# Performance work log

Hardware: AMD Instinct MI355X
Metric: run time of the kernel (lower is better)

## Reference

```python
import jax, jax.numpy as jnp
import numpy as np

SEQ, H, NC = 20, 128, 100000

def _lstm_cell(x, h, c, Wih, Whh, bih, bhh):
    # gates: [B, 4H] in PyTorch order i, f, g, o
    g = x @ Wih.T + bih + h @ Whh.T + bhh
    i, f, gg, o = jnp.split(g, 4, axis=-1)
    c2 = jax.nn.sigmoid(f) * c + jax.nn.sigmoid(i) * jnp.tanh(gg)
    h2 = jax.nn.sigmoid(o) * jnp.tanh(c2)
    return h2, c2

def setup_inputs() -> dict:
    key = jax.random.key(0)
    ks = jax.random.split(key, 24)
    u = lambda k, shp, bound: jax.random.uniform(k, shp, jnp.float32, -bound, bound)
    s1 = 1.0 / np.sqrt(H)       # PyTorch LSTMCell init bound, hidden_size=H
    s2 = 1.0 / np.sqrt(2 * H)   # combined cell, hidden_size=2H
    kn = lambda k, shp: jax.random.normal(k, shp, jnp.float32) * np.sqrt(2.0 / shp[1])  # kaiming_normal_
    return {
        'x': jax.random.normal(ks[0], (SEQ, 1, H), jnp.float32),
        'h0f': kn(ks[1], (1, H)), 'c0f': kn(ks[2], (1, H)),
        'h0b': kn(ks[3], (1, H)), 'c0b': kn(ks[4], (1, H)),
        'h0l': kn(ks[5], (1, 2 * H)), 'c0l': kn(ks[6], (1, 2 * H)),
        'Wih_f': u(ks[7], (4 * H, H), s1), 'Whh_f': u(ks[8], (4 * H, H), s1),
        'bih_f': u(ks[9], (4 * H,), s1), 'bhh_f': u(ks[10], (4 * H,), s1),
        'Wih_b': u(ks[11], (4 * H, H), s1), 'Whh_b': u(ks[12], (4 * H, H), s1),
        'bih_b': u(ks[13], (4 * H,), s1), 'bhh_b': u(ks[14], (4 * H,), s1),
        'Wih_l': u(ks[15], (8 * H, 2 * H), s2), 'Whh_l': u(ks[16], (8 * H, 2 * H), s2),
        'bih_l': u(ks[17], (8 * H,), s2), 'bhh_l': u(ks[18], (8 * H,), s2),
        'Wlin': u(ks[19], (NC, 2 * H), 1.0 / np.sqrt(2 * H)),
        'blin': u(ks[20], (NC,), 1.0 / np.sqrt(2 * H)),
    }

def reference(x, h0f, c0f, h0b, c0b, h0l, c0l,
              Wih_f, Whh_f, bih_f, bhh_f,
              Wih_b, Whh_b, bih_b, bhh_b,
              Wih_l, Whh_l, bih_l, bhh_l,
              Wlin, blin):
    xs = x.reshape(SEQ, 1, H)

    def step_f(carry, xt):
        h, c = _lstm_cell(xt, carry[0], carry[1], Wih_f, Whh_f, bih_f, bhh_f)
        return (h, c), h
    _, fwd = jax.lax.scan(step_f, (h0f, c0f), xs)          # [SEQ, 1, H]

    def step_b(carry, xt):
        h, c = _lstm_cell(xt, carry[0], carry[1], Wih_b, Whh_b, bih_b, bhh_b)
        return (h, c), h
    # backward list is kept in reversed-scan order (NOT flipped back), per source zip
    _, bwd = jax.lax.scan(step_b, (h0b, c0b), xs[::-1])    # [SEQ, 1, H]

    comb = jnp.concatenate([fwd, bwd], axis=-1)            # [SEQ, 1, 2H]

    def step_l(carry, xt):
        h, c = _lstm_cell(xt, carry[0], carry[1], Wih_l, Whh_l, bih_l, bhh_l)
        return (h, c), h
    _, hl = jax.lax.scan(step_l, (h0l, c0l), comb)         # [SEQ, 1, 2H]

    fb = hl.reshape(SEQ, 2 * H)
    return fb @ Wlin.T + blin                              # [SEQ, NC]
```

## Files before the change

### kernel.cpp

```cpp
#include <hip/hip_runtime.h>
#include <stdint.h>

#define SEQ  20
#define H1   128
#define H2   256
#define NCLS 100000

__device__ __forceinline__ float sigm(float x) { return 1.0f / (1.0f + __expf(-x)); }
__device__ __forceinline__ float tanhfast(float x) {
    float e = __expf(-2.0f * fabsf(x));
    float t = (1.0f - e) / (1.0f + e);
    return copysignf(t, x);
}

__device__ __forceinline__ void gbar(int* cnt, int target) {
    __syncthreads();
    if (threadIdx.x == 0) {
        __hip_atomic_fetch_add(cnt, 1, __ATOMIC_ACQ_REL, __HIP_MEMORY_SCOPE_AGENT);
        while (__hip_atomic_load(cnt, __ATOMIC_ACQUIRE, __HIP_MEMORY_SCOPE_AGENT) < target)
            __builtin_amdgcn_s_sleep(2);
    }
    __syncthreads();
}

__global__ __launch_bounds__(256, 1) void k_l1g(
    const float* __restrict__ x,
    const float* __restrict__ h0f, const float* __restrict__ c0f,
    const float* __restrict__ h0b, const float* __restrict__ c0b,
    const float* __restrict__ WihF, const float* __restrict__ WhhF,
    const float* __restrict__ bihF, const float* __restrict__ bhhF,
    const float* __restrict__ WihB, const float* __restrict__ WhhB,
    const float* __restrict__ bihB, const float* __restrict__ bhhB,
    float* __restrict__ comb,
    float* __restrict__ hg,
    int* __restrict__ sync)
{
    const int b   = blockIdx.x;
    const int dir = b >> 3, sub = b & 7;
    const float* Wih = dir ? WihB : WihF;
    const float* Whh = dir ? WhhB : WhhF;
    const float* bih = dir ? bihB : bihF;
    const float* bhh = dir ? bhhB : bhhF;
    const float* h0  = dir ? h0b  : h0f;
    const float* c0  = dir ? c0b  : c0f;

    __shared__ float whhS[64 * 129];
    __shared__ float gxs[64][SEQ];
    __shared__ float xs[H1];
    __shared__ float partial[4 * 64];
    __shared__ float hcur[H1];
    __shared__ float gv[64];

    const int tid = threadIdx.x;
    const int lr  = tid & 63;
    const int q   = tid >> 6;

    float biasv = 0.0f;
    if (tid < 64) {
        int R = (tid >> 4) * H1 + sub * 16 + (tid & 15);
        biasv = bih[R] + bhh[R];
    }
    {
        int r2 = tid >> 2, sg = tid & 3;
        int R = (r2 >> 4) * H1 + sub * 16 + (r2 & 15);
        const float* src = Whh + R * H1 + sg * 32;
        float* dst = whhS + r2 * 129 + sg * 32;
        for (int i = 0; i < 32; ++i) dst[i] = src[i];
    }
    if (tid < H1) hcur[tid] = h0[tid];
    float cst = 0.0f;
    if (tid < 16) cst = c0[sub * 16 + tid];
    __syncthreads();

    for (int t = 0; t < SEQ; ++t) {
        int tx = dir ? (SEQ - 1 - t) : t;
        if (tid < H1) xs[tid] = x[tx * H1 + tid];
        __syncthreads();
        {
            int R = (lr >> 4) * H1 + sub * 16 + (lr & 15);
            const float* wp = Wih + R * H1 + q * 32;
            const float* xp = xs + q * 32;
            float a = 0.0f;
#pragma unroll
            for (int k = 0; k < 32; k += 4) {
                float4 wv = *(const float4*)(wp + k);
                a += wv.x * xp[k] + wv.y * xp[k + 1] + wv.z * xp[k + 2] + wv.w * xp[k + 3];
            }
            partial[q * 64 + lr] = a;
        }
        __syncthreads();
        if (tid < 64)
            gxs[tid][t] = biasv + partial[tid] + partial[64 + tid]
                        + partial[128 + tid] + partial[192 + tid];
        __syncthreads();
    }

    for (int t = 0; t < SEQ; ++t) {
        {
            const float* wp = whhS + lr * 129 + q * 32;
            const float* hp = hcur + q * 32;
            float a = 0.0f;
#pragma unroll
            for (int k = 0; k < 32; ++k) a += wp[k] * hp[k];
            partial[q * 64 + lr] = a;
        }
        __syncthreads();
        if (tid < 64)
            gv[tid] = gxs[tid][t] + partial[tid] + partial[64 + tid]
                    + partial[128 + tid] + partial[192 + tid];
        __syncthreads();
        if (tid < 16) {
            float gi = gv[tid], gf = gv[16 + tid], gg = gv[32 + tid], go = gv[48 + tid];
            float cn = sigm(gf) * cst + sigm(gi) * tanhfast(gg);
            cst = cn;
            float hn = sigm(go) * tanhfast(cn);
            comb[t * H2 + dir * H1 + sub * 16 + tid] = hn;
            __hip_atomic_store(&hg[dir * H1 + sub * 16 + tid], hn,
                               __ATOMIC_RELEASE, __HIP_MEMORY_SCOPE_AGENT);
        }
        gbar(&sync[dir], 8 * (t + 1));
        if (tid < H1)
            hcur[tid] = __hip_atomic_load(&hg[dir * H1 + tid],
                                          __ATOMIC_RELAXED, __HIP_MEMORY_SCOPE_AGENT);
        __syncthreads();
    }
}

__global__ __launch_bounds__(256, 1) void k_l2g(
    const float* __restrict__ Whhl,
    const float* __restrict__ h0l, const float* __restrict__ c0l,
    const float* __restrict__ Wihl,
    const float* __restrict__ bihl, const float* __restrict__ bhhl,
    const float* __restrict__ comb,
    float* __restrict__ fb,
    float* __restrict__ hg2,
    int* __restrict__ sync)
{
    const int b = blockIdx.x;
    __shared__ float whhS[32 * 257];
    __shared__ float gxs[32][SEQ];
    __shared__ float combt[H2];
    __shared__ float partial[8 * 32];
    __shared__ float hcur[H2];
    __shared__ float gv[32];

    const int tid = threadIdx.x;
    const int lr  = tid & 31;
    const int q   = tid >> 5;
    const int c0  = b * 8;

    float biasv = 0.0f;
    if (tid < 32) {
        int R = (tid >> 3) * H2 + c0 + (tid & 7);
        biasv = bihl[R] + bhhl[R];
    }
    {
        int r2 = tid >> 3, sg = tid & 7;
        int R = (r2 >> 3) * H2 + c0 + (r2 & 7);
        const float* src = Whhl + R * H2 + sg * 32;
        float* dst = whhS + r2 * 257 + sg * 32;
        for (int i = 0; i < 32; ++i) dst[i] = src[i];
    }
    if (tid < H2) hcur[tid] = h0l[tid];
    float cst = 0.0f;
    if (tid < 8) cst = c0l[c0 + tid];
    __syncthreads();

    for (int t = 0; t < SEQ; ++t) {
        combt[tid] = comb[t * H2 + tid];
        __syncthreads();
        {
            int R = (lr >> 3) * H2 + c0 + (lr & 7);
            const float* wp = Wihl + R * H2 + q * 32;
            const float* cp = combt + q * 32;
            float a = 0.0f;
#pragma unroll
            for (int k = 0; k < 32; k += 4) {
                float4 wv = *(const float4*)(wp + k);
                a += wv.x * cp[k] + wv.y * cp[k + 1] + wv.z * cp[k + 2] + wv.w * cp[k + 3];
            }
            partial[q * 32 + lr] = a;
        }
        __syncthreads();
        if (tid < 32) {
            float s = biasv;
#pragma unroll
            for (int qq = 0; qq < 8; ++qq) s += partial[qq * 32 + tid];
            gxs[tid][t] = s;
        }
        __syncthreads();
    }

    for (int t = 0; t < SEQ; ++t) {
        {
            const float* wp = whhS + lr * 257 + q * 32;
            const float* hp = hcur + q * 32;
            float a = 0.0f;
#pragma unroll
            for (int k = 0; k < 32; ++k) a += wp[k] * hp[k];
            partial[q * 32 + lr] = a;
        }
        __syncthreads();
        if (tid < 32) {
            float s = gxs[tid][t];
#pragma unroll
            for (int qq = 0; qq < 8; ++qq) s += partial[qq * 32 + tid];
            gv[tid] = s;
        }
        __syncthreads();
        if (tid < 8) {
            float gi = gv[tid], gf = gv[8 + tid], gg = gv[16 + tid], go = gv[24 + tid];
            float cn = sigm(gf) * cst + sigm(gi) * tanhfast(gg);
            cst = cn;
            float hn = sigm(go) * tanhfast(cn);
            fb[t * H2 + c0 + tid] = hn;
            __hip_atomic_store(&hg2[c0 + tid], hn,
                               __ATOMIC_RELEASE, __HIP_MEMORY_SCOPE_AGENT);
        }
        gbar(&sync[2], 32 * (t + 1));
        hcur[tid] = __hip_atomic_load(&hg2[tid],
                                      __ATOMIC_RELAXED, __HIP_MEMORY_SCOPE_AGENT);
        __syncthreads();
    }
}

__global__ __launch_bounds__(256, 4) void k_out_v(
    const float* __restrict__ Wlin, const float* __restrict__ blin,
    const float* __restrict__ fb, float* __restrict__ out)
{
    __shared__ float fbs[H2][SEQ];
    const int tid = threadIdx.x;
    for (int t = 0; t < SEQ; ++t) fbs[tid][t] = fb[t * H2 + tid];
    __syncthreads();

    int n = blockIdx.x * 256 + tid;
    if (n >= NCLS) return;
    float acc[SEQ];
    float bv = blin[n];
#pragma unroll
    for (int t = 0; t < SEQ; ++t) acc[t] = bv;

    const float* wp = Wlin + (size_t)n * H2;
    for (int k = 0; k < H2; k += 4) {
        float4 wv = *(const float4*)(wp + k);
#pragma unroll
        for (int t = 0; t < SEQ; t += 4) {
            float4 f0 = *(const float4*)(&fbs[k][t]);
            float4 f1 = *(const float4*)(&fbs[k + 1][t]);
            float4 f2 = *(const float4*)(&fbs[k + 2][t]);
            float4 f3 = *(const float4*)(&fbs[k + 3][t]);
            acc[t]     += wv.x * f0.x + wv.y * f1.x + wv.z * f2.x + wv.w * f3.x;
            acc[t + 1] += wv.x * f0.y + wv.y * f1.y + wv.z * f2.y + wv.w * f3.y;
            acc[t + 2] += wv.x * f0.z + wv.y * f1.z + wv.z * f2.z + wv.w * f3.z;
            acc[t + 3] += wv.x * f0.w + wv.y * f1.w + wv.z * f2.w + wv.w * f3.w;
        }
    }
#pragma unroll
    for (int t = 0; t < SEQ; ++t)
        out[(size_t)t * NCLS + n] = acc[t];
}

extern "C" void kernel_launch(void* const* d_in, const int* in_sizes, int n_in,
                              void* d_out, int out_size, void* d_ws, size_t ws_size,
                              hipStream_t stream)
{
    const float* x    = (const float*)d_in[0];
    const float* h0f_ = (const float*)d_in[1];
    const float* c0f_ = (const float*)d_in[2];
    const float* h0b_ = (const float*)d_in[3];
    const float* c0b_ = (const float*)d_in[4];
    const float* h0l_ = (const float*)d_in[5];
    const float* c0l_ = (const float*)d_in[6];
    const float* WihF = (const float*)d_in[7];
    const float* WhhF = (const float*)d_in[8];
    const float* bihF = (const float*)d_in[9];
    const float* bhhF = (const float*)d_in[10];
    const float* WihB = (const float*)d_in[11];
    const float* WhhB = (const float*)d_in[12];
    const float* bihB = (const float*)d_in[13];
    const float* bhhB = (const float*)d_in[14];
    const float* Wihl = (const float*)d_in[15];
    const float* Whhl = (const float*)d_in[16];
    const float* bihl = (const float*)d_in[17];
    const float* bhhl = (const float*)d_in[18];
    const float* Wlin = (const float*)d_in[19];
    const float* blin = (const float*)d_in[20];

    char* ws = (char*)d_ws;
    int*   sync = (int*)ws;
    float* hg   = (float*)(ws + 256);
    float* hg2  = (float*)(ws + 1536);
    float* comb = (float*)(ws + 4096);
    float* fb   = (float*)(ws + 24576);

    hipMemsetAsync(sync, 0, 256, stream);

    k_l1g<<<16, 256, 0, stream>>>(x, h0f_, c0f_, h0b_, c0b_,
                                  WihF, WhhF, bihF, bhhF,
                                  WihB, WhhB, bihB, bhhB,
                                  comb, hg, sync);
    k_l2g<<<32, 256, 0, stream>>>(Whhl, h0l_, c0l_,
                                  Wihl, bihl, bhhl,
                                  comb, fb, hg2, sync);
    k_out_v<<<391, 256, 0, stream>>>(Wlin, blin, fb, (float*)d_out);
}
```

Measured before the change: 358.0 us.

## Collapse LSTM layers to fewer blocks with register-resident weights

```diff
diff --git a/kernel.cpp b/kernel.cpp
--- a/kernel.cpp
+++ b/kernel.cpp
@@ -18,12 +18,12 @@
     if (threadIdx.x == 0) {
         __hip_atomic_fetch_add(cnt, 1, __ATOMIC_ACQ_REL, __HIP_MEMORY_SCOPE_AGENT);
         while (__hip_atomic_load(cnt, __ATOMIC_ACQUIRE, __HIP_MEMORY_SCOPE_AGENT) < target)
-            __builtin_amdgcn_s_sleep(2);
-    }
-    __syncthreads();
-}
-
-__global__ __launch_bounds__(256, 1) void k_l1g(
+            __builtin_amdgcn_s_sleep(1);
+    }
+    __syncthreads();
+}
+
+__global__ __launch_bounds__(512, 2) void k_l1r(
     const float* __restrict__ x,
     const float* __restrict__ h0f, const float* __restrict__ c0f,
     const float* __restrict__ h0b, const float* __restrict__ c0b,
@@ -31,12 +31,9 @@
     const float* __restrict__ bihF, const float* __restrict__ bhhF,
     const float* __restrict__ WihB, const float* __restrict__ WhhB,
     const float* __restrict__ bihB, const float* __restrict__ bhhB,
-    float* __restrict__ comb,
-    float* __restrict__ hg,
-    int* __restrict__ sync)
-{
-    const int b   = blockIdx.x;
-    const int dir = b >> 3, sub = b & 7;
+    float* __restrict__ comb)
+{
+    const int dir = blockIdx.x;
     const float* Wih = dir ? WihB : WihF;
     const float* Whh = dir ? WhhB : WhhF;
     const float* bih = dir ? bihB : bihF;
@@ -44,89 +41,73 @@
     const float* h0  = dir ? h0b  : h0f;
     const float* c0  = dir ? c0b  : c0f;
 
-    __shared__ float whhS[64 * 129];
-    __shared__ float gxs[64][SEQ];
-    __shared__ float xs[H1];
-    __shared__ float partial[4 * 64];
+    __shared__ float xs[SEQ * H1];
     __shared__ float hcur[H1];
-    __shared__ float gv[64];
+    __shared__ float gv[4 * H1];
+    __shared__ float gxs[4 * H1][SEQ + 1];
 
     const int tid = threadIdx.x;
-    const int lr  = tid & 63;
-    const int q   = tid >> 6;
-
-    float biasv = 0.0f;
-    if (tid < 64) {
-        int R = (tid >> 4) * H1 + sub * 16 + (tid & 15);
-        biasv = bih[R] + bhh[R];
-    }
-    {
-        int r2 = tid >> 2, sg = tid & 3;
-        int R = (r2 >> 4) * H1 + sub * 16 + (r2 & 15);
-        const float* src = Whh + R * H1 + sg * 32;
-        float* dst = whhS + r2 * 129 + sg * 32;
-        for (int i = 0; i < 32; ++i) dst[i] = src[i];
-    }
+
+    for (int i = tid; i < SEQ * H1; i += 512) xs[i] = x[i];
     if (tid < H1) hcur[tid] = h0[tid];
-    float cst = 0.0f;
-    if (tid < 16) cst = c0[sub * 16 + tid];
-    __syncthreads();
-
-    for (int t = 0; t < SEQ; ++t) {
-        int tx = dir ? (SEQ - 1 - t) : t;
-        if (tid < H1) xs[tid] = x[tx * H1 + tid];
-        __syncthreads();
-        {
-            int R = (lr >> 4) * H1 + sub * 16 + (lr & 15);
-            const float* wp = Wih + R * H1 + q * 32;
-            const float* xp = xs + q * 32;
-            float a = 0.0f;
-#pragma unroll
-            for (int k = 0; k < 32; k += 4) {
-                float4 wv = *(const float4*)(wp + k);
-                a += wv.x * xp[k] + wv.y * xp[k + 1] + wv.z * xp[k + 2] + wv.w * xp[k + 3];
-            }
-            partial[q * 64 + lr] = a;
-        }
-        __syncthreads();
-        if (tid < 64)
-            gxs[tid][t] = biasv + partial[tid] + partial[64 + tid]
-                        + partial[128 + tid] + partial[192 + tid];
-        __syncthreads();
-    }
-
-    for (int t = 0; t < SEQ; ++t) {
-        {
-            const float* wp = whhS + lr * 129 + q * 32;
-            const float* hp = hcur + q * 32;
-            float a = 0.0f;
-#pragma unroll
-            for (int k = 0; k < 32; ++k) a += wp[k] * hp[k];
-            partial[q * 64 + lr] = a;
-        }
-        __syncthreads();
-        if (tid < 64)
-            gv[tid] = gxs[tid][t] + partial[tid] + partial[64 + tid]
-                    + partial[128 + tid] + partial[192 + tid];
-        __syncthreads();
-        if (tid < 16) {
-            float gi = gv[tid], gf = gv[16 + tid], gg = gv[32 + tid], go = gv[48 + tid];
-            float cn = sigm(gf) * cst + sigm(gi) * tanhfast(gg);
-            cst = cn;
+    float creg = (tid < H1) ? c0[tid] : 0.0f;
+    const float bias = bih[tid] + bhh[tid];
+
+    float w[H1];
+    {
+        const float* wr = Wih + tid * H1;
+#pragma unroll
+        for (int k = 0; k < H1; k += 4) {
+            float4 v = *(const float4*)(wr + k);
+            w[k] = v.x; w[k + 1] = v.y; w[k + 2] = v.z; w[k + 3] = v.w;
+        }
+    }
+    __syncthreads();
+
+    for (int t = 0; t < SEQ; ++t) {
+        const float* xp = xs + (dir ? (SEQ - 1 - t) : t) * H1;
+        float a0 = 0.f, a1 = 0.f, a2 = 0.f, a3 = 0.f;
+#pragma unroll
+        for (int k = 0; k < H1; k += 4) {
+            float4 hv = *(const float4*)(xp + k);
+            a0 += w[k] * hv.x; a1 += w[k + 1] * hv.y;
+            a2 += w[k + 2] * hv.z; a3 += w[k + 3] * hv.w;
+        }
+        gxs[tid][t] = bias + ((a0 + a1) + (a2 + a3));
+    }
+
+    {
+        const float* wr = Whh + tid * H1;
+#pragma unroll
+        for (int k = 0; k < H1; k += 4) {
+            float4 v = *(const float4*)(wr + k);
+            w[k] = v.x; w[k + 1] = v.y; w[k + 2] = v.z; w[k + 3] = v.w;
+        }
+    }
+
+    for (int t = 0; t < SEQ; ++t) {
+        float a0 = 0.f, a1 = 0.f, a2 = 0.f, a3 = 0.f;
+#pragma unroll
+        for (int k = 0; k < H1; k += 4) {
+            float4 hv = *(const float4*)(hcur + k);
+            a0 += w[k] * hv.x; a1 += w[k + 1] * hv.y;
+            a2 += w[k + 2] * hv.z; a3 += w[k + 3] * hv.w;
+        }
+        gv[tid] = gxs[tid][t] + ((a0 + a1) + (a2 + a3));
+        __syncthreads();
+        if (tid < H1) {
+            float gi = gv[tid], gf = gv[H1 + tid], gg = gv[2 * H1 + tid], go = gv[3 * H1 + tid];
+            float cn = sigm(gf) * creg + sigm(gi) * tanhfast(gg);
+            creg = cn;
             float hn = sigm(go) * tanhfast(cn);
-            comb[t * H2 + dir * H1 + sub * 16 + tid] = hn;
-            __hip_atomic_store(&hg[dir * H1 + sub * 16 + tid], hn,
-                               __ATOMIC_RELEASE, __HIP_MEMORY_SCOPE_AGENT);
-        }
-        gbar(&sync[dir], 8 * (t + 1));
-        if (tid < H1)
-            hcur[tid] = __hip_atomic_load(&hg[dir * H1 + tid],
-                                          __ATOMIC_RELAXED, __HIP_MEMORY_SCOPE_AGENT);
-        __syncthreads();
-    }
-}
-
-__global__ __launch_bounds__(256, 1) void k_l2g(
+            comb[t * H2 + dir * H1 + tid] = hn;
+            hcur[tid] = hn;
+        }
+        __syncthreads();
+    }
+}
+
+__global__ __launch_bounds__(512, 2) void k_l2r(
     const float* __restrict__ Whhl,
     const float* __restrict__ h0l, const float* __restrict__ c0l,
     const float* __restrict__ Wihl,
@@ -137,89 +118,81 @@
     int* __restrict__ sync)
 {
     const int b = blockIdx.x;
-    __shared__ float whhS[32 * 257];
-    __shared__ float gxs[32][SEQ];
-    __shared__ float combt[H2];
-    __shared__ float partial[8 * 32];
+    __shared__ float cs[SEQ * H2];
     __shared__ float hcur[H2];
-    __shared__ float gv[32];
-
-    const int tid = threadIdx.x;
-    const int lr  = tid & 31;
-    const int q   = tid >> 5;
-    const int c0  = b * 8;
-
-    float biasv = 0.0f;
-    if (tid < 32) {
-        int R = (tid >> 3) * H2 + c0 + (tid & 7);
-        biasv = bihl[R] + bhhl[R];
-    }
-    {
-        int r2 = tid >> 3, sg = tid & 7;
-        int R = (r2 >> 3) * H2 + c0 + (r2 & 7);
-        const float* src = Whhl + R * H2 + sg * 32;
-        float* dst = whhS + r2 * 257 + sg * 32;
-        for (int i = 0; i < 32; ++i) dst[i] = src[i];
-    }
+    __shared__ float gv[4 * 64];
+    __shared__ float gxs[H2][SEQ + 1];
+
+    const int tid  = threadIdx.x;
+    const int L    = tid >> 1;
+    const int half = tid & 1;
+    const int R    = (L >> 6) * H2 + b * 64 + (L & 63);
+    const float bias = bihl[R] + bhhl[R];
+
+    for (int i = tid; i < SEQ * H2; i += 512) cs[i] = comb[i];
     if (tid < H2) hcur[tid] = h0l[tid];
-    float cst = 0.0f;
-    if (tid < 8) cst = c0l[c0 + tid];
-    __syncthreads();
-
-    for (int t = 0; t < SEQ; ++t) {
-        combt[tid] = comb[t * H2 + tid];
-        __syncthreads();
-        {
-            int R = (lr >> 3) * H2 + c0 + (lr & 7);
-            const float* wp = Wihl + R * H2 + q * 32;
-            const float* cp = combt + q * 32;
-            float a = 0.0f;
-#pragma unroll
-            for (int k = 0; k < 32; k += 4) {
-                float4 wv = *(const float4*)(wp + k);
-                a += wv.x * cp[k] + wv.y * cp[k + 1] + wv.z * cp[k + 2] + wv.w * cp[k + 3];
-            }
-            partial[q * 32 + lr] = a;
-        }
-        __syncthreads();
-        if (tid < 32) {
-            float s = biasv;
-#pragma unroll
-            for (int qq = 0; qq < 8; ++qq) s += partial[qq * 32 + tid];
-            gxs[tid][t] = s;
-        }
-        __syncthreads();
-    }
-
-    for (int t = 0; t < SEQ; ++t) {
-        {
-            const float* wp = whhS + lr * 257 + q * 32;
-            const float* hp = hcur + q * 32;
-            float a = 0.0f;
-#pragma unroll
-            for (int k = 0; k < 32; ++k) a += wp[k] * hp[k];
-            partial[q * 32 + lr] = a;
-        }
-        __syncthreads();
-        if (tid < 32) {
-            float s = gxs[tid][t];
-#pragma unroll
-            for (int qq = 0; qq < 8; ++qq) s += partial[qq * 32 + tid];
-            gv[tid] = s;
-        }
-        __syncthreads();
-        if (tid < 8) {
-            float gi = gv[tid], gf = gv[8 + tid], gg = gv[16 + tid], go = gv[24 + tid];
-            float cn = sigm(gf) * cst + sigm(gi) * tanhfast(gg);
-            cst = cn;
+    float creg = (tid < 64) ? c0l[b * 64 + tid] : 0.0f;
+
+    float w[H1];
+    {
+        const float* wr = Wihl + R * H2 + half * H1;
+#pragma unroll
+        for (int k = 0; k < H1; k += 4) {
+            float4 v = *(const float4*)(wr + k);
+            w[k] = v.x; w[k + 1] = v.y; w[k + 2] = v.z; w[k + 3] = v.w;
+        }
+    }
+    __syncthreads();
+
+    for (int t = 0; t < SEQ; ++t) {
+        const float* cp = cs + t * H2 + half * H1;
+        float a0 = 0.f, a1 = 0.f, a2 = 0.f, a3 = 0.f;
+#pragma unroll
+        for (int k = 0; k < H1; k += 4) {
+            float4 hv = *(const float4*)(cp + k);
+            a0 += w[k] * hv.x; a1 += w[k + 1] * hv.y;
+            a2 += w[k + 2] * hv.z; a3 += w[k + 3] * hv.w;
+        }
+        float a = (a0 + a1) + (a2 + a3);
+        a += __shfl_xor(a, 1);
+        if (half == 0) gxs[L][t] = bias + a;
+    }
+
+    {
+        const float* wr = Whhl + R * H2 + half * H1;
+#pragma unroll
+        for (int k = 0; k < H1; k += 4) {
+            float4 v = *(const float4*)(wr + k);
+            w[k] = v.x; w[k + 1] = v.y; w[k + 2] = v.z; w[k + 3] = v.w;
+        }
+    }
+
+    for (int t = 0; t < SEQ; ++t) {
+        const float* hp = hcur + half * H1;
+        float a0 = 0.f, a1 = 0.f, a2 = 0.f, a3 = 0.f;
+#pragma unroll
+        for (int k = 0; k < H1; k += 4) {
+            float4 hv = *(const float4*)(hp + k);
+            a0 += w[k] * hv.x; a1 += w[k + 1] * hv.y;
+            a2 += w[k + 2] * hv.z; a3 += w[k + 3] * hv.w;
+        }
+        float a = (a0 + a1) + (a2 + a3);
+        a += __shfl_xor(a, 1);
+        if (half == 0) gv[L] = gxs[L][t] + a;
+        __syncthreads();
+        if (tid < 64) {
+            float gi = gv[tid], gf = gv[64 + tid], gg = gv[128 + tid], go = gv[192 + tid];
+            float cn = sigm(gf) * creg + sigm(gi) * tanhfast(gg);
+            creg = cn;
             float hn = sigm(go) * tanhfast(cn);
-            fb[t * H2 + c0 + tid] = hn;
-            __hip_atomic_store(&hg2[c0 + tid], hn,
+            fb[t * H2 + b * 64 + tid] = hn;
+            __hip_atomic_store(&hg2[b * 64 + tid], hn,
                                __ATOMIC_RELEASE, __HIP_MEMORY_SCOPE_AGENT);
         }
-        gbar(&sync[2], 32 * (t + 1));
-        hcur[tid] = __hip_atomic_load(&hg2[tid],
-                                      __ATOMIC_RELAXED, __HIP_MEMORY_SCOPE_AGENT);
+        gbar(&sync[0], 4 * (t + 1));
+        if (tid < H2)
+            hcur[tid] = __hip_atomic_load(&hg2[tid],
+                                          __ATOMIC_RELAXED, __HIP_MEMORY_SCOPE_AGENT);
         __syncthreads();
     }
 }
@@ -288,19 +261,18 @@
 
     char* ws = (char*)d_ws;
     int*   sync = (int*)ws;
-    float* hg   = (float*)(ws + 256);
     float* hg2  = (float*)(ws + 1536);
     float* comb = (float*)(ws + 4096);
     float* fb   = (float*)(ws + 24576);
 
     hipMemsetAsync(sync, 0, 256, stream);
 
-    k_l1g<<<16, 256, 0, stream>>>(x, h0f_, c0f_, h0b_, c0b_,
-                                  WihF, WhhF, bihF, bhhF,
-                                  WihB, WhhB, bihB, bhhB,
-                                  comb, hg, sync);
-    k_l2g<<<32, 256, 0, stream>>>(Whhl, h0l_, c0l_,
-                                  Wihl, bihl, bhhl,
-                                  comb, fb, hg2, sync);
+    k_l1r<<<2, 512, 0, stream>>>(x, h0f_, c0f_, h0b_, c0b_,
+                                 WihF, WhhF, bihF, bhhF,
+                                 WihB, WhhB, bihB, bhhB,
+                                 comb);
+    k_l2r<<<4, 512, 0, stream>>>(Whhl, h0l_, c0l_,
+                                 Wihl, bihl, bhhl,
+                                 comb, fb, hg2, sync);
     k_out_v<<<391, 256, 0, stream>>>(Wlin, blin, fb, (float*)d_out);
 }
```

Result: slower. 397.8 us (+11.1%).
